# Performance work log

Measured on AMD Instinct MI355X. Metric: run time of the kernel, lower is better.

## Reference

```python
import jax, jax.numpy as jnp
import numpy as np

DIM = 300
VOCAB = 50000
B = 16
T_ART = 2000   # divisible by lcm(1,2,4,10,25)=100 -> no remainder branch in ContractExpand
T_Q = 30
T_OPT = 16
RANGES = (1, 2, 4, 10, 25)


def setup_inputs():
    key = jax.random.key(0)
    ks = jax.random.split(key, 32)
    s = 1.0 / np.sqrt(DIM)
    n = lambda i, shape, scale: jax.random.normal(ks[i], shape, jnp.float32) * scale
    return {
        "option1_in": jax.random.randint(ks[0], (B, T_OPT), 0, VOCAB),
        "option2_in": jax.random.randint(ks[1], (B, T_OPT), 0, VOCAB),
        "option3_in": jax.random.randint(ks[2], (B, T_OPT), 0, VOCAB),
        "option4_in": jax.random.randint(ks[3], (B, T_OPT), 0, VOCAB),
        "question_in": jax.random.randint(ks[4], (B, T_Q), 0, VOCAB),
        "article_in": jax.random.randint(ks[5], (B, T_ART), 0, VOCAB),
        "emb": n(6, (VOCAB, DIM), 0.1),
        # ContractExpand: 5 range-specific DIM->DIM linears
        "ce_W": n(7, (5, DIM, DIM), s),
        "ce_b": n(8, (5, DIM), 0.01),
        # MultiRangedReasoning gate mixers: 5->3 and 3->1
        "mr1_W": n(9, (3, 5), 0.4),
        "mr1_b": n(10, (3,), 0.01),
        "mr2_W": n(11, (1, 3), 0.05),   # small scale keeps gate < 1 so 2000-step scan is stable
        "mr2_b": jnp.zeros((1,), jnp.float32),
        # MRU encoding linears
        "Wz": n(12, (DIM, DIM), s), "bz": n(13, (DIM,), 0.01),
        "Wo": n(14, (DIM, DIM), s), "bo": n(15, (DIM,), 0.01),
        # BiAttention key projections
        "f1_W": n(16, (DIM, DIM), s), "f1_b": n(17, (DIM,), 0.01),
        "f2_W": n(18, (DIM, DIM), s), "f2_b": n(19, (DIM,), 0.01),
        "f3_W": n(20, (DIM, DIM), s), "f3_b": n(21, (DIM,), 0.01),
        # AnswerSelection: 2*DIM -> DIM/4 -> 1
        "as1_W": n(22, (DIM // 4, 2 * DIM), 1.0 / np.sqrt(2 * DIM)),
        "as1_b": n(23, (DIM // 4,), 0.01),
        "as2_W": n(24, (1, DIM // 4), 1.0 / np.sqrt(DIM // 4)),
        "as2_b": n(25, (1,), 0.01),
    }


def _attention(main, attn_in, W, b):
    # score[b,t,w] = (W @ attn_in[b,w] + b) . main[b,t]; softmax over w; mix attn_in
    keys = attn_in @ W.T + b                               # (B,Tw,D)
    probs = jax.nn.softmax(jnp.einsum('btd,bwd->btw', main, keys), axis=-1)
    return jnp.einsum('btw,bwd->btd', probs, attn_in)      # (B,Tt,D)


def _forward(option1_in, option2_in, option3_in, option4_in, question_in, article_in,
             emb, ce_W, ce_b, mr1_W, mr1_b, mr2_W, mr2_b, Wz, bz, Wo, bo,
             f1_W, f1_b, f2_W, f2_b, f3_W, f3_b, as1_W, as1_b, as2_W, as2_b):
    art = emb[article_in]                                  # (B,T,D)
    q = emb[question_in]                                   # (B,Tq,D)
    opts = [emb[o] for o in (option1_in, option2_in, option3_in, option4_in)]

    # --- MultiRangedReasoning gate ---
    blocks = []
    for i, r in enumerate(RANGES):
        g = T_ART // r
        xs = art.reshape(B, g, r, DIM).sum(2)              # group-sum over r consecutive words
        h = jax.nn.relu(jnp.einsum('bgd,ed->bge', xs, ce_W[i]) + ce_b[i])
        blocks.append(jnp.repeat(h, r, axis=1) / r)        # expand back to (B,T,D)
    Y = jnp.stack(blocks, axis=-1)                         # (B,T,D,5)
    h1 = jax.nn.relu(jnp.einsum('btdr,kr->btdk', Y, mr1_W) + mr1_b)
    gate = jax.nn.relu(jnp.einsum('btdk,ok->btdo', h1, mr2_W) + mr2_b)[..., 0]  # (B,T,D)

    # --- MRU encoding: c_t = g_t*c_{t-1} + (1-g_t)*z_t ; h_t = o_t*c_t ---
    z = jnp.tanh(art @ Wz.T + bz)
    o = jnp.tanh(art @ Wo.T + bo)

    def step(c, gz):
        g_t, z_t = gz
        c = g_t * c + (1.0 - g_t) * z_t
        return c, c

    _, cs = jax.lax.scan(step, jnp.zeros((B, DIM), art.dtype),
                         (gate.transpose(1, 0, 2), z.transpose(1, 0, 2)))
    art_enc = o * cs.transpose(1, 0, 2)                    # (B,T,D)

    # --- bi-attention + per-option answer vector ---
    aoq = _attention(art_enc, q, f1_W, f1_b)               # article on question
    vecs = []
    for opt in opts:
        aoqo = _attention(aoq, opt, f2_W, f2_b)            # (B,T,D)
        ooa = _attention(aoq, opt, f3_W, f3_b)             # (B,T,D)
        vecs.append(jnp.concatenate([aoqo.mean(1), ooa.mean(1)], axis=-1))  # (B,2D)
    ans = jnp.stack(vecs, 0)                               # (4,B,2D)

    h = jax.nn.relu(ans @ as1_W.T + as1_b)                 # (4,B,75)
    scores = (h @ as2_W.T + as2_b)[..., 0]                 # (4,B)
    return scores.T                                        # (B,4)


def reference(option1_in, option2_in, option3_in, option4_in, question_in, article_in,
              emb, ce_W, ce_b, mr1_W, mr1_b, mr2_W, mr2_b, Wz, bz, Wo, bo,
              f1_W, f1_b, f2_W, f2_b, f3_W, f3_b, as1_W, as1_b, as2_W, as2_b):
    return _forward(option1_in, option2_in, option3_in, option4_in, question_in, article_in,
                    emb, ce_W, ce_b, mr1_W, mr1_b, mr2_W, mr2_b, Wz, bz, Wo, bo,
                    f1_W, f1_b, f2_W, f2_b, f3_W, f3_b, as1_W, as1_b, as2_W, as2_b)
```

## Files before the change

kernel.cpp:

```cpp
#include <hip/hip_runtime.h>
#include <math.h>

typedef unsigned short ushortT;
typedef short bf8 __attribute__((ext_vector_type(8)));
typedef float f32x4 __attribute__((ext_vector_type(4)));
typedef unsigned short us4 __attribute__((ext_vector_type(4)));

__device__ __forceinline__ float bf2f(ushortT u){
    union { unsigned int i; float f; } v; v.i = ((unsigned int)u) << 16; return v.f;
}
__device__ __forceinline__ ushortT f2bf(float f){
    union { float f; unsigned int i; } v; v.f = f;
    unsigned int x = v.i;
    return (ushortT)((x + 0x7fffu + ((x >> 16) & 1u)) >> 16);
}
__device__ __forceinline__ float4 f4add(float4 a, float4 b){
    return make_float4(a.x + b.x, a.y + b.y, a.z + b.z, a.w + b.w);
}


constexpr size_t OFF_ART   = 0;
constexpr size_t OFF_R2    = 9600000;
constexpr size_t OFF_GATE  = 19200000;
constexpr size_t OFF_HC    = 28800000;
constexpr size_t OFF_WB    = 37344000;
constexpr size_t OFF_QEMB  = 38316800;
constexpr size_t OFF_KEYSQ = 38460800;
constexpr size_t OFF_OPTE  = 38604800;
constexpr size_t OFF_KEYS2 = 38912000;
constexpr size_t OFF_KEYS3 = 39219200;
constexpr size_t OFF_SCANA = 39526400;
constexpr size_t OFF_SCANB = 39718400;
constexpr size_t OFF_CST   = 39910400;
constexpr size_t OFF_PART  = 40102400;
constexpr size_t OFF_MALL  = 40231424;



__global__ void k_pack(float* ws, const float* ceW, const float* Wz, const float* Wo,
                       const float* f1W, const float* f2W, const float* f3W){
    int id = blockIdx.x * 256 + threadIdx.x;
    if (id >= 972800) return;
    int m = id / 97280; int rr = id % 97280;
    int kt = rr / 9728; rr %= 9728;
    int nt = rr / 512;  rr %= 512;
    int lane = rr / 8; int j = rr % 8;
    int d = kt * 32 + (lane >> 4) * 8 + j;
    int e = nt * 16 + (lane & 15);
    float w = 0.f;
    if (d < 300 && e < 300) {
        const float* src = (m < 5) ? (ceW + (size_t)m * 90000)
                         : (m == 5) ? Wz : (m == 6) ? Wo
                         : (m == 7) ? f1W : (m == 8) ? f2W : f3W;
        w = src[(size_t)e * 300 + d];
    }
    ushortT hi = f2bf(w);
    ushortT lo = f2bf(w - bf2f(hi));
    ushortT* wb = (ushortT*)(ws + OFF_WB);
    wb[((size_t)(m * 20 + kt) * 19 + nt) * 512 + lane * 8 + j] = hi;
    wb[((size_t)(m * 20 + 10 + kt) * 19 + nt) * 512 + lane * 8 + j] = lo;
}

__device__ __forceinline__ bf8 load_bfrag(const ushortT* wb, int mp, int kt, int nt, int lane){
    return *(const bf8*)(wb + (((size_t)(mp + kt) * 19 + nt) * 512 + lane * 8));
}
__device__ __forceinline__ bf8 lds_afrag(const ushortT* LA, int tile, int kt, int part, int lane){
    return *(const bf8*)(LA + ((tile * 10 + kt) * 2 + part) * 512 + lane * 8);
}
__device__ __forceinline__ void lds_store_split(ushortT* LA, int r, int dc4, float4 s){
    int kt = dc4 / 8;
    int kk = (dc4 % 8) * 4;
    int quad = kk / 8, j = kk % 8;
    int lane = quad * 16 + (r & 15), tile = r >> 4;
    us4 h, l;
    h.x = f2bf(s.x); l.x = f2bf(s.x - bf2f(h.x));
    h.y = f2bf(s.y); l.y = f2bf(s.y - bf2f(h.y));
    h.z = f2bf(s.z); l.z = f2bf(s.z - bf2f(h.z));
    h.w = f2bf(s.w); l.w = f2bf(s.w - bf2f(h.w));
    int base = ((tile * 10 + kt) * 2) * 512 + lane * 8 + j;
    *(us4*)&LA[base] = h;
    *(us4*)&LA[base + 512] = l;
}
__device__ __forceinline__ void lds_zero_kt9(ushortT* LA, int tid){
    for (int i = tid; i < 1024; i += 256) {
        int sl = i >> 8, u = i & 255;
        int slice = (sl < 2) ? (18 + sl) : (36 + sl);
        *(unsigned int*)&LA[slice * 512 + u * 2] = 0u;
    }
}

__global__ __launch_bounds__(320) void k_gather2(float* ws, const float* emb,
                         const int* art_in, const int* q_in,
                         const int* o1, const int* o2, const int* o3, const int* o4){
    int gb = blockIdx.x, tid = threadIdx.x;
    const float4* embv = (const float4*)emb;
    if (gb < 160) {
        if (tid >= 300) return;
        int b = gb / 10, c = gb % 10;
        int rg = tid / 75, d4 = tid % 75;
        int tbase = c * 200 + rg * 50;
        float4 s2 = make_float4(0.f,0.f,0.f,0.f), s5 = s2;
        float4* artv  = (float4*)(ws + OFF_ART);
        float4* s2v   = (float4*)(ws + OFF_GATE);
        float4* s5v   = (float4*)(ws + OFF_R2);
        for (int i = 0; i < 50; i++) {
            int t = tbase + i;
            int tok = art_in[b * 2000 + t];
            float4 v = embv[(size_t)tok * 75 + d4];
            artv[((size_t)b * 2000 + t) * 75 + d4] = v;
            s2 = f4add(s2, v); s5 = f4add(s5, v);
            if ((i & 1) == 1) { s2v[((size_t)b * 1000 + (t >> 1)) * 75 + d4] = s2; s2 = make_float4(0.f,0.f,0.f,0.f); }
            if (i % 5 == 4)   { s5v[((size_t)b * 400 + t / 5) * 75 + d4] = s5;   s5 = make_float4(0.f,0.f,0.f,0.f); }
        }
    } else {
        int id = (gb - 160) * 320 + tid;
        if (id < 36000) {
            size_t row = id / 75; int wi = id % 75;
            ((float4*)(ws + OFF_QEMB))[id] = embv[(size_t)q_in[row] * 75 + wi];
        } else if (id < 112800) {
            int i3 = id - 36000; size_t row = i3 / 75; int wi = i3 % 75;
            int opt = (int)(row / 256); int rr = (int)(row % 256);
            const int* op = (opt == 0) ? o1 : (opt == 1) ? o2 : (opt == 2) ? o3 : o4;
            ((float4*)(ws + OFF_OPTE))[i3] = embv[(size_t)op[rr] * 75 + wi];
        }
    }
}

__global__ __launch_bounds__(256) void k_ce_coarse(float* ws, const float* ceb){
    int gb = blockIdx.x;
    int kind, rows0, wi, rowLocal0;
    if (gb < 40)       { kind = 3; rows0 = 27200; wi = 4; rowLocal0 = gb * 32; }
    else if (gb < 140) { kind = 2; rows0 = 24000; wi = 3; rowLocal0 = (gb - 40) * 32; }
    else if (gb < 390) { kind = 1; rows0 = 16000; wi = 2; rowLocal0 = (gb - 140) * 32; }
    else               { kind = 0; rows0 = 0;     wi = 1; rowLocal0 = (gb - 390) * 32; }

    __shared__ ushortT LA[20480];
    int tid = threadIdx.x;
    lds_zero_kt9(LA, tid);
    __syncthreads();
    const float4* S2v = (const float4*)(ws + OFF_GATE);
    const float4* S5v = (const float4*)(ws + OFF_R2);
    for (int v = tid; v < 2400; v += 256) {
        int r = v / 75, dc4 = v % 75;
        int R = rowLocal0 + r;
        float4 s;
        if (kind == 0) {
            s = S2v[(size_t)R * 75 + dc4];
        } else if (kind == 1) {
            int b = R / 500, g = R % 500;
            const float4* p = S2v + ((size_t)b * 1000 + 2 * g) * 75 + dc4;
            s = f4add(p[0], p[75]);
        } else if (kind == 2) {
            int b = R / 200, g = R % 200;
            const float4* p = S5v + ((size_t)b * 400 + 2 * g) * 75 + dc4;
            s = f4add(p[0], p[75]);
        } else {
            int b = R / 80, g = R % 80;
            const float4* p = S5v + ((size_t)b * 400 + 5 * g) * 75 + dc4;
            s = f4add(f4add(p[0], p[75]), f4add(p[150], p[225]));
            s = f4add(s, p[300]);
        }
        lds_store_split(LA, r, dc4, s);
    }
    __syncthreads();

    int lane = tid & 63, wv = tid >> 6;
    int mrow = lane & 15, quad = lane >> 4;
    const ushortT* wb = (const ushortT*)(ws + OFF_WB);
    int mpH = wi * 20, mpL = wi * 20 + 10;

    for (int p = 0; p < 5; p++) {
        int nt = wv + p * 4; if (nt >= 19) break;
        f32x4 a0 = {0.f,0.f,0.f,0.f}, a1 = {0.f,0.f,0.f,0.f};
        #pragma unroll
        for (int kt = 0; kt < 10; kt++) {
            bf8 Ah0 = lds_afrag(LA, 0, kt, 0, lane), Al0 = lds_afrag(LA, 0, kt, 1, lane);
            bf8 Ah1 = lds_afrag(LA, 1, kt, 0, lane), Al1 = lds_afrag(LA, 1, kt, 1, lane);
            bf8 Bh = load_bfrag(wb, mpH, kt, nt, lane);
            bf8 Bl = load_bfrag(wb, mpL, kt, nt, lane);
            a0 = __builtin_amdgcn_mfma_f32_16x16x32_bf16(Ah0, Bh, a0, 0, 0, 0);
            a1 = __builtin_amdgcn_mfma_f32_16x16x32_bf16(Ah1, Bh, a1, 0, 0, 0);
            a0 = __builtin_amdgcn_mfma_f32_16x16x32_bf16(Ah0, Bl, a0, 0, 0, 0);
            a1 = __builtin_amdgcn_mfma_f32_16x16x32_bf16(Ah1, Bl, a1, 0, 0, 0);
            a0 = __builtin_amdgcn_mfma_f32_16x16x32_bf16(Al0, Bh, a0, 0, 0, 0);
            a1 = __builtin_amdgcn_mfma_f32_16x16x32_bf16(Al1, Bh, a1, 0, 0, 0);
        }
        int e = nt * 16 + mrow;
        if (e < 300) {
            float bv = ceb[wi * 300 + e];
            #pragma unroll
            for (int q = 0; q < 4; q++) {
                int r0 = rows0 + rowLocal0 + quad * 4 + q;
                ws[OFF_HC + (size_t)r0 * 300 + e] = fmaxf(a0[q] + bv, 0.f);
                ws[OFF_HC + (size_t)(r0 + 16) * 300 + e] = fmaxf(a1[q] + bv, 0.f);
            }
        }
    }
}

__global__ __launch_bounds__(256) void k_fused(float* ws, const float* ceb,
                                               const float* m1W, const float* m1b,
                                               const float* m2W, const float* m2b,
                                               const float* bz, const float* bo){
    int row0 = blockIdx.x * 32;
    __shared__ ushortT LA[20480];
    int tid = threadIdx.x;
    lds_zero_kt9(LA, tid);
    __syncthreads();
    for (int v = tid; v < 2400; v += 256) {
        int r = v / 75, dc4 = v % 75;
        float4 s = *(const float4*)&ws[OFF_ART + (size_t)(row0 + r) * 300 + dc4 * 4];
        lds_store_split(LA, r, dc4, s);
    }
    __syncthreads();

    float w1[3][5], b1[3], w2[3], b2;
    #pragma unroll
    for (int k = 0; k < 3; k++) {
        #pragma unroll
        for (int i = 0; i < 5; i++) w1[k][i] = m1W[k * 5 + i];
        b1[k] = m1b[k]; w2[k] = m2W[k];
    }
    b2 = m2b[0];

    int lane = tid & 63, wv = tid >> 6;
    int mrow = lane & 15, quad = lane >> 4;
    const ushortT* wb = (const ushortT*)(ws + OFF_WB);

    for (int p = 0; p < 5; p++) {
        int nt = wv + p * 4; if (nt >= 19) break;
        f32x4 aA0 = {0.f,0.f,0.f,0.f}, aA1 = aA0;
        f32x4 aZ0 = aA0, aZ1 = aA0, aO0 = aA0, aO1 = aA0;
        #pragma unroll
        for (int kt = 0; kt < 10; kt++) {
            bf8 Ah0 = lds_afrag(LA, 0, kt, 0, lane), Al0 = lds_afrag(LA, 0, kt, 1, lane);
            bf8 Ah1 = lds_afrag(LA, 1, kt, 0, lane), Al1 = lds_afrag(LA, 1, kt, 1, lane);
            bf8 BAh = load_bfrag(wb, 0,   kt, nt, lane);
            bf8 BAl = load_bfrag(wb, 10,  kt, nt, lane);
            bf8 BZh = load_bfrag(wb, 100, kt, nt, lane);
            bf8 BZl = load_bfrag(wb, 110, kt, nt, lane);
            bf8 BOh = load_bfrag(wb, 120, kt, nt, lane);
            bf8 BOl = load_bfrag(wb, 130, kt, nt, lane);
            aA0 = __builtin_amdgcn_mfma_f32_16x16x32_bf16(Ah0, BAh, aA0, 0, 0, 0);
            aZ0 = __builtin_amdgcn_mfma_f32_16x16x32_bf16(Ah0, BZh, aZ0, 0, 0, 0);
            aO0 = __builtin_amdgcn_mfma_f32_16x16x32_bf16(Ah0, BOh, aO0, 0, 0, 0);
            aA1 = __builtin_amdgcn_mfma_f32_16x16x32_bf16(Ah1, BAh, aA1, 0, 0, 0);
            aZ1 = __builtin_amdgcn_mfma_f32_16x16x32_bf16(Ah1, BZh, aZ1, 0, 0, 0);
            aO1 = __builtin_amdgcn_mfma_f32_16x16x32_bf16(Ah1, BOh, aO1, 0, 0, 0);
            aA0 = __builtin_amdgcn_mfma_f32_16x16x32_bf16(Ah0, BAl, aA0, 0, 0, 0);
            aZ0 = __builtin_amdgcn_mfma_f32_16x16x32_bf16(Ah0, BZl, aZ0, 0, 0, 0);
            aO0 = __builtin_amdgcn_mfma_f32_16x16x32_bf16(Ah0, BOl, aO0, 0, 0, 0);
            aA1 = __builtin_amdgcn_mfma_f32_16x16x32_bf16(Ah1, BAl, aA1, 0, 0, 0);
            aZ1 = __builtin_amdgcn_mfma_f32_16x16x32_bf16(Ah1, BZl, aZ1, 0, 0, 0);
            aO1 = __builtin_amdgcn_mfma_f32_16x16x32_bf16(Ah1, BOl, aO1, 0, 0, 0);
            aA0 = __builtin_amdgcn_mfma_f32_16x16x32_bf16(Al0, BAh, aA0, 0, 0, 0);
            aZ0 = __builtin_amdgcn_mfma_f32_16x16x32_bf16(Al0, BZh, aZ0, 0, 0, 0);
            aO0 = __builtin_amdgcn_mfma_f32_16x16x32_bf16(Al0, BOh, aO0, 0, 0, 0);
            aA1 = __builtin_amdgcn_mfma_f32_16x16x32_bf16(Al1, BAh, aA1, 0, 0, 0);
            aZ1 = __builtin_amdgcn_mfma_f32_16x16x32_bf16(Al1, BZh, aZ1, 0, 0, 0);
            aO1 = __builtin_amdgcn_mfma_f32_16x16x32_bf16(Al1, BOh, aO1, 0, 0, 0);
        }
        int e = nt * 16 + mrow;
        if (e < 300) {
            float cebe = ceb[e], bze = bz[e], boe = bo[e];
            #pragma unroll
            for (int tile = 0; tile < 2; tile++) {
                #pragma unroll
                for (int q = 0; q < 4; q++) {
                    float vA = tile ? aA1[q] : aA0[q];
                    float vZ = tile ? aZ1[q] : aZ0[q];
                    float vO = tile ? aO1[q] : aO0[q];
                    int row = row0 + tile * 16 + quad * 4 + q;
                    int bb = row / 2000, t = row % 2000;
                    size_t c1 = OFF_HC + ((size_t)bb * 1000 + t / 2) * 300;
                    size_t c2 = OFF_HC + (16000 + (size_t)bb * 500 + t / 4) * 300;
                    size_t c3 = OFF_HC + (24000 + (size_t)bb * 200 + t / 10) * 300;
                    size_t c4 = OFF_HC + (27200 + (size_t)bb * 80 + t / 25) * 300;
                    float y0 = fmaxf(vA + cebe, 0.f);
                    float y1 = ws[c1 + e] * 0.5f;
                    float y2 = ws[c2 + e] * 0.25f;
                    float y3 = ws[c3 + e] * 0.1f;
                    float y4 = ws[c4 + e] * 0.04f;
                    float gacc = b2;
                    #pragma unroll
                    for (int k = 0; k < 3; k++) {
                        float a = b1[k] + y0 * w1[k][0] + y1 * w1[k][1] + y2 * w1[k][2]
                                + y3 * w1[k][3] + y4 * w1[k][4];
                        gacc += fmaxf(a, 0.f) * w2[k];
                    }
                    ws[OFF_GATE + (size_t)row * 300 + e] = fmaxf(gacc, 0.f);
                    ws[OFF_R2 + (size_t)row * 300 + e] = tanhf(vZ + bze);
                    ws[OFF_ART + (size_t)row * 300 + e] = tanhf(vO + boe);
                }
            }
        }
    }
}

__global__ void k_scan1(float* ws){
    int tid = blockIdx.x * 256 + threadIdx.x;
    if (tid >= 192000) return;
    int c = tid / 4800, ch = tid % 4800;
    int b = ch / 300, d = ch % 300;
    size_t base = (size_t)b * 2000 * 300 + d;
    float A = 1.f, Bv = 0.f;
    int t0 = c * 50;
    for (int k = 0; k < 50; k++) {
        size_t ix = base + (size_t)(t0 + k) * 300;
        float g = ws[OFF_GATE + ix], zz = ws[OFF_R2 + ix];
        Bv = g * Bv + (1.f - g) * zz;
        A *= g;
    }
    ws[OFF_SCANA + tid] = A;
    ws[OFF_SCANB + tid] = Bv;
}

__global__ void k_scan2(float* ws){
    int ch = blockIdx.x * 256 + threadIdx.x;
    if (ch >= 4800) return;
    float c = 0.f;
    for (int j = 0; j < 40; j++) {
        ws[OFF_CST + (size_t)j * 4800 + ch] = c;
        c = ws[OFF_SCANA + (size_t)j * 4800 + ch] * c + ws[OFF_SCANB + (size_t)j * 4800 + ch];
    }
}

__global__ void k_scan3(float* ws){
    int tid = blockIdx.x * 256 + threadIdx.x;
    if (tid >= 192000) return;
    int c = tid / 4800, ch = tid % 4800;
    int b = ch / 300, d = ch % 300;
    size_t base = (size_t)b * 2000 * 300 + d;
    float cc = ws[OFF_CST + tid];
    int t0 = c * 50;
    for (int k = 0; k < 50; k++) {
        size_t ix = base + (size_t)(t0 + k) * 300;
        float g = ws[OFF_GATE + ix], zz = ws[OFF_R2 + ix];
        cc = g * cc + (1.f - g) * zz;
        ws[OFF_R2 + ix] = ws[OFF_ART + ix] * cc;
    }
}

__global__ __launch_bounds__(256) void k_keysm(float* ws, const float* f1b,
                                               const float* f2b, const float* f3b){
    int gb = blockIdx.x;
    int wm, rowLocal0; size_t inoff, outoff; const float* bias;
    if (gb < 15)      { wm = 7; inoff = OFF_QEMB; outoff = OFF_KEYSQ; bias = f1b; rowLocal0 = gb * 32; }
    else if (gb < 47) { wm = 8; inoff = OFF_OPTE; outoff = OFF_KEYS2; bias = f2b; rowLocal0 = (gb - 15) * 32; }
    else              { wm = 9; inoff = OFF_OPTE; outoff = OFF_KEYS3; bias = f3b; rowLocal0 = (gb - 47) * 32; }

    __shared__ ushortT LA[20480];
    int tid = threadIdx.x;
    lds_zero_kt9(LA, tid);
    __syncthreads();
    for (int v = tid; v < 2400; v += 256) {
        int r = v / 75, dc4 = v % 75;
        float4 s = *(const float4*)&ws[inoff + (size_t)(rowLocal0 + r) * 300 + dc4 * 4];
        lds_store_split(LA, r, dc4, s);
    }
    __syncthreads();

    int lane = tid & 63, wv = tid >> 6;
    int mrow = lane & 15, quad = lane >> 4;
    const ushortT* wb = (const ushortT*)(ws + OFF_WB);
    int mpH = wm * 20, mpL = wm * 20 + 10;

    for (int p = 0; p < 5; p++) {
        int nt = wv + p * 4; if (nt >= 19) break;
        f32x4 a0 = {0.f,0.f,0.f,0.f}, a1 = {0.f,0.f,0.f,0.f};
        #pragma unroll
        for (int kt = 0; kt < 10; kt++) {
            bf8 Ah0 = lds_afrag(LA, 0, kt, 0, lane), Al0 = lds_afrag(LA, 0, kt, 1, lane);
            bf8 Ah1 = lds_afrag(LA, 1, kt, 0, lane), Al1 = lds_afrag(LA, 1, kt, 1, lane);
            bf8 Bh = load_bfrag(wb, mpH, kt, nt, lane);
            bf8 Bl = load_bfrag(wb, mpL, kt, nt, lane);
            a0 = __builtin_amdgcn_mfma_f32_16x16x32_bf16(Ah0, Bh, a0, 0, 0, 0);
            a1 = __builtin_amdgcn_mfma_f32_16x16x32_bf16(Ah1, Bh, a1, 0, 0, 0);
            a0 = __builtin_amdgcn_mfma_f32_16x16x32_bf16(Ah0, Bl, a0, 0, 0, 0);
            a1 = __builtin_amdgcn_mfma_f32_16x16x32_bf16(Ah1, Bl, a1, 0, 0, 0);
            a0 = __builtin_amdgcn_mfma_f32_16x16x32_bf16(Al0, Bh, a0, 0, 0, 0);
            a1 = __builtin_amdgcn_mfma_f32_16x16x32_bf16(Al1, Bh, a1, 0, 0, 0);
        }
        int e = nt * 16 + mrow;
        if (e < 300) {
            float bv = bias[e];
            #pragma unroll
            for (int q = 0; q < 4; q++) {
                int r0 = rowLocal0 + quad * 4 + q;
                ws[outoff + (size_t)r0 * 300 + e] = a0[q] + bv;
                ws[outoff + (size_t)(r0 + 16) * 300 + e] = a1[q] + bv;
            }
        }
    }
}

__global__ __launch_bounds__(256) void k_matt(float* ws){
    int b = blockIdx.x;
    __shared__ float Q[30 * 300];
    int tid = threadIdx.x;
    for (int v = tid; v < 2250; v += 256)
        *(float4*)&Q[v * 4] = *(const float4*)&ws[OFF_QEMB + (size_t)b * 9000 + (size_t)v * 4];
    __syncthreads();
    int cw = tid & 127, half = tid >> 7;
    int combo = cw >> 4, w = cw & 15;
    size_t kbase = (combo < 4)
        ? OFF_KEYS2 + ((size_t)combo * 256 + (size_t)b * 16 + w) * 300
        : OFF_KEYS3 + ((size_t)(combo - 4) * 256 + (size_t)b * 16 + w) * 300;
    const float4* kr = (const float4*)&ws[kbase];
    for (int wp = half * 15; wp < half * 15 + 15; wp++) {
        const float4* qr = (const float4*)&Q[wp * 300];
        float a = 0.f;
        #pragma unroll 5
        for (int j = 0; j < 75; j++) {
            float4 k = kr[j], q = qr[j];
            a += k.x * q.x + k.y * q.y + k.z * q.z + k.w * q.w;
        }
        ws[OFF_MALL + (size_t)b * 3840 + (size_t)wp * 128 + cw] = a;
    }
}

__global__ __launch_bounds__(256) void k_attn(float* ws){
    int tile = blockIdx.x, b = blockIdx.y;
    int t0 = tile * 32;
    __shared__ __align__(16) float U[9728];
    __shared__ float S[32 * 30];
    int tid = threadIdx.x;

    for (int v = tid; v < 2432; v += 256) {
        int r = v / 76, c = v % 76;
        int t = t0 + r;
        float4 val = make_float4(0.f, 0.f, 0.f, 0.f);
        if (c < 75 && t < 2000)
            val = *(const float4*)&ws[OFF_R2 + ((size_t)b * 2000 + t) * 300 + (size_t)c * 4];
        *(float4*)&U[r * 304 + c * 4] = val;
    }
    __syncthreads();

    if (tid < 240) {
        int q = tid / 30, w = tid % 30;
        const float4* kr = (const float4*)&ws[OFF_KEYSQ + (size_t)b * 9000 + (size_t)w * 300];
        const float4* x0 = (const float4*)&U[(q * 4 + 0) * 304];
        const float4* x1 = (const float4*)&U[(q * 4 + 1) * 304];
        const float4* x2 = (const float4*)&U[(q * 4 + 2) * 304];
        const float4* x3 = (const float4*)&U[(q * 4 + 3) * 304];
        float a0 = 0.f, a1 = 0.f, a2 = 0.f, a3 = 0.f;
        #pragma unroll 5
        for (int j = 0; j < 75; j++) {
            float4 k = kr[j];
            float4 v0 = x0[j], v1 = x1[j], v2 = x2[j], v3 = x3[j];
            a0 += v0.x * k.x + v0.y * k.y + v0.z * k.z + v0.w * k.w;
            a1 += v1.x * k.x + v1.y * k.y + v1.z * k.z + v1.w * k.w;
            a2 += v2.x * k.x + v2.y * k.y + v2.z * k.z + v2.w * k.w;
            a3 += v3.x * k.x + v3.y * k.y + v3.z * k.z + v3.w * k.w;
        }
        S[(q * 4 + 0) * 30 + w] = a0;
        S[(q * 4 + 1) * 30 + w] = a1;
        S[(q * 4 + 2) * 30 + w] = a2;
        S[(q * 4 + 3) * 30 + w] = a3;
    }
    __syncthreads();

    for (int v = tid; v < 960; v += 256)
        *(float4*)&U[v * 4] = *(const float4*)&ws[OFF_MALL + (size_t)b * 3840 + (size_t)v * 4];
    if (tid < 32) {
        float m = -1e30f;
        for (int w = 0; w < 30; w++) m = fmaxf(m, S[tid * 30 + w]);
        float s = 0.f;
        for (int w = 0; w < 30; w++) { float e = expf(S[tid * 30 + w] - m); S[tid * 30 + w] = e; s += e; }
        float inv = 1.f / s;
        for (int w = 0; w < 30; w++) S[tid * 30 + w] *= inv;
    }
    __syncthreads();

    {
        int c = tid >> 5, tl = tid & 31;
        float v[16];
        #pragma unroll
        for (int w = 0; w < 16; w++) v[w] = 0.f;
        for (int wp = 0; wp < 30; wp++) {
            float p1 = S[tl * 30 + wp];
            const float* Mr = &U[wp * 128 + c * 16];
            #pragma unroll
            for (int w = 0; w < 16; w++) v[w] += p1 * Mr[w];
        }
        float mx = v[0];
        #pragma unroll
        for (int w = 1; w < 16; w++) mx = fmaxf(mx, v[w]);
        float sum = 0.f;
        #pragma unroll
        for (int w = 0; w < 16; w++) { v[w] = expf(v[w] - mx); sum += v[w]; }
        float inv = ((t0 + tl) < 2000) ? (1.f / sum) : 0.f;
        #pragma unroll
        for (int w = 0; w < 16; w += 4) {
            float4 o = make_float4(v[w] * inv, v[w+1] * inv, v[w+2] * inv, v[w+3] * inv);
            *(float4*)&U[4224 + tl * 132 + c * 16 + w] = o;
        }
    }
    __syncthreads();

    if (tid < 128) {
        int combo = tid >> 4, w = tid & 15;
        float s = 0.f;
        for (int r = 0; r < 32; r++) s += U[4224 + r * 132 + tid];
        ws[OFF_PART + (((size_t)combo * 16 + b) * 63 + tile) * 16 + w] = s;
    }
}

__global__ __launch_bounds__(256) void k_final(float* ws, const float* as1W, const float* as1b,
                                               const float* as2W, const float* as2b, float* out){
    int blk = blockIdx.x; int o = blk >> 4, b = blk & 15;
    __shared__ float vec[600]; __shared__ float cm[32]; __shared__ float hb[80];
    int tid = threadIdx.x;
    if (tid < 32) {
        int half = tid / 16, wk = tid % 16;
        int combo = half ? (4 + o) : o;
        float s = 0.f;
        size_t base = OFF_PART + (((size_t)combo * 16 + b) * 63) * 16 + wk;
        for (int t = 0; t < 63; t++) s += ws[base + (size_t)t * 16];
        cm[tid] = s * (1.f / 2000.f);
    }
    __syncthreads();
    const float* oe = ws + OFF_OPTE + ((size_t)o * 256 + (size_t)b * 16) * 300;
    for (int idx = tid; idx < 600; idx += 256) {
        int half = idx / 300, e = idx % 300;
        float acc = 0.f;
        for (int w = 0; w < 16; w++) acc += cm[half * 16 + w] * oe[(size_t)w * 300 + e];
        vec[idx] = acc;
    }
    __syncthreads();
    if (tid < 75) {
        float acc = as1b[tid];
        for (int m = 0; m < 600; m++) acc += vec[m] * as1W[(size_t)tid * 600 + m];
        hb[tid] = fmaxf(acc, 0.f);
    }
    __syncthreads();
    if (tid == 0) {
        float s = as2b[0];
        for (int j = 0; j < 75; j++) s += hb[j] * as2W[j];
        out[b * 4 + o] = s;
    }
}

extern "C" void kernel_launch(void* const* d_in, const int* in_sizes, int n_in,
                              void* d_out, int out_size, void* d_ws, size_t ws_size,
                              hipStream_t stream) {
    float* ws = (float*)d_ws;
    const int* o1 = (const int*)d_in[0];
    const int* o2 = (const int*)d_in[1];
    const int* o3 = (const int*)d_in[2];
    const int* o4 = (const int*)d_in[3];
    const int* qin = (const int*)d_in[4];
    const int* ain = (const int*)d_in[5];
    const float* emb  = (const float*)d_in[6];
    const float* ceW  = (const float*)d_in[7];
    const float* ceb  = (const float*)d_in[8];
    const float* m1W  = (const float*)d_in[9];
    const float* m1b  = (const float*)d_in[10];
    const float* m2W  = (const float*)d_in[11];
    const float* m2b  = (const float*)d_in[12];
    const float* Wz   = (const float*)d_in[13];
    const float* bz   = (const float*)d_in[14];
    const float* Wo   = (const float*)d_in[15];
    const float* bo   = (const float*)d_in[16];
    const float* f1W  = (const float*)d_in[17];
    const float* f1b  = (const float*)d_in[18];
    const float* f2W  = (const float*)d_in[19];
    const float* f2b  = (const float*)d_in[20];
    const float* f3W  = (const float*)d_in[21];
    const float* f3b  = (const float*)d_in[22];
    const float* as1W = (const float*)d_in[23];
    const float* as1b = (const float*)d_in[24];
    const float* as2W = (const float*)d_in[25];
    const float* as2b = (const float*)d_in[26];

    k_pack<<<3800, 256, 0, stream>>>(ws, ceW, Wz, Wo, f1W, f2W, f3W);
    k_gather2<<<513, 320, 0, stream>>>(ws, emb, ain, qin, o1, o2, o3, o4);
    k_ce_coarse<<<890, 256, 0, stream>>>(ws, ceb);
    k_fused<<<1000, 256, 0, stream>>>(ws, ceb, m1W, m1b, m2W, m2b, bz, bo);
    k_scan1<<<750, 256, 0, stream>>>(ws);
    k_scan2<<<19, 256, 0, stream>>>(ws);
    k_scan3<<<750, 256, 0, stream>>>(ws);
    k_keysm<<<79, 256, 0, stream>>>(ws, f1b, f2b, f3b);
    k_matt<<<16, 256, 0, stream>>>(ws);
    k_attn<<<dim3(63, 16), 256, 0, stream>>>(ws);
    k_final<<<64, 256, 0, stream>>>(ws, as1W, as1b, as2W, as2b, (float*)d_out);
}
```

Before: 539.1 us.

## Fuse scan apply into attention load, regather embeddings, finer scan chunks

The third scan pass is removed. k_attn now recomputes the recurrence for its own 32-step tile, starting from the carried state written by scan2, and multiplies by the output gate while filling shared memory. The article-embedding copy written by the gather kernel is dropped, and k_fused reads embedding rows directly through the token ids instead. Scan chunks shrink from 50 to 16 steps so that each attention tile (two chunks) lines up with a chunk boundary, and more threads run in scan1. In exchange, scan2 walks a longer serial chain, and the attention fill loop is serial over 32 timesteps with strided global loads from only 300 threads per block.

```diff
diff --git a/kernel.cpp b/kernel.cpp
--- a/kernel.cpp
+++ b/kernel.cpp
@@ -30,10 +30,10 @@
 constexpr size_t OFF_KEYS2 = 38912000;
 constexpr size_t OFF_KEYS3 = 39219200;
 constexpr size_t OFF_SCANA = 39526400;
-constexpr size_t OFF_SCANB = 39718400;
-constexpr size_t OFF_CST   = 39910400;
-constexpr size_t OFF_PART  = 40102400;
-constexpr size_t OFF_MALL  = 40231424;
+constexpr size_t OFF_SCANB = 40126400;
+constexpr size_t OFF_CST   = 40726400;
+constexpr size_t OFF_PART  = 41326400;
+constexpr size_t OFF_MALL  = 41455424;
 
 
 
@@ -100,14 +100,12 @@
         int rg = tid / 75, d4 = tid % 75;
         int tbase = c * 200 + rg * 50;
         float4 s2 = make_float4(0.f,0.f,0.f,0.f), s5 = s2;
-        float4* artv  = (float4*)(ws + OFF_ART);
-        float4* s2v   = (float4*)(ws + OFF_GATE);
-        float4* s5v   = (float4*)(ws + OFF_R2);
+        float4* s2v = (float4*)(ws + OFF_GATE);
+        float4* s5v = (float4*)(ws + OFF_R2);
         for (int i = 0; i < 50; i++) {
             int t = tbase + i;
             int tok = art_in[b * 2000 + t];
             float4 v = embv[(size_t)tok * 75 + d4];
-            artv[((size_t)b * 2000 + t) * 75 + d4] = v;
             s2 = f4add(s2, v); s5 = f4add(s5, v);
             if ((i & 1) == 1) { s2v[((size_t)b * 1000 + (t >> 1)) * 75 + d4] = s2; s2 = make_float4(0.f,0.f,0.f,0.f); }
             if (i % 5 == 4)   { s5v[((size_t)b * 400 + t / 5) * 75 + d4] = s5;   s5 = make_float4(0.f,0.f,0.f,0.f); }
@@ -198,7 +196,8 @@
     }
 }
 
-__global__ __launch_bounds__(256) void k_fused(float* ws, const float* ceb,
+__global__ __launch_bounds__(256) void k_fused(float* ws, const float* emb, const int* art_in,
+                                               const float* ceb,
                                                const float* m1W, const float* m1b,
                                                const float* m2W, const float* m2b,
                                                const float* bz, const float* bo){
@@ -207,9 +206,11 @@
     int tid = threadIdx.x;
     lds_zero_kt9(LA, tid);
     __syncthreads();
+    const float4* embv = (const float4*)emb;
     for (int v = tid; v < 2400; v += 256) {
         int r = v / 75, dc4 = v % 75;
-        float4 s = *(const float4*)&ws[OFF_ART + (size_t)(row0 + r) * 300 + dc4 * 4];
+        int tok = art_in[row0 + r];
+        float4 s = embv[(size_t)tok * 75 + dc4];
         lds_store_split(LA, r, dc4, s);
     }
     __syncthreads();
@@ -299,13 +300,13 @@
 
 __global__ void k_scan1(float* ws){
     int tid = blockIdx.x * 256 + threadIdx.x;
-    if (tid >= 192000) return;
+    if (tid >= 600000) return;
     int c = tid / 4800, ch = tid % 4800;
     int b = ch / 300, d = ch % 300;
     size_t base = (size_t)b * 2000 * 300 + d;
     float A = 1.f, Bv = 0.f;
-    int t0 = c * 50;
-    for (int k = 0; k < 50; k++) {
+    int t0 = c * 16;
+    for (int k = 0; k < 16; k++) {
         size_t ix = base + (size_t)(t0 + k) * 300;
         float g = ws[OFF_GATE + ix], zz = ws[OFF_R2 + ix];
         Bv = g * Bv + (1.f - g) * zz;
@@ -319,25 +320,9 @@
     int ch = blockIdx.x * 256 + threadIdx.x;
     if (ch >= 4800) return;
     float c = 0.f;
-    for (int j = 0; j < 40; j++) {
+    for (int j = 0; j < 125; j++) {
         ws[OFF_CST + (size_t)j * 4800 + ch] = c;
         c = ws[OFF_SCANA + (size_t)j * 4800 + ch] * c + ws[OFF_SCANB + (size_t)j * 4800 + ch];
-    }
-}
-
-__global__ void k_scan3(float* ws){
-    int tid = blockIdx.x * 256 + threadIdx.x;
-    if (tid >= 192000) return;
-    int c = tid / 4800, ch = tid % 4800;
-    int b = ch / 300, d = ch % 300;
-    size_t base = (size_t)b * 2000 * 300 + d;
-    float cc = ws[OFF_CST + tid];
-    int t0 = c * 50;
-    for (int k = 0; k < 50; k++) {
-        size_t ix = base + (size_t)(t0 + k) * 300;
-        float g = ws[OFF_GATE + ix], zz = ws[OFF_R2 + ix];
-        cc = g * cc + (1.f - g) * zz;
-        ws[OFF_R2 + ix] = ws[OFF_ART + ix] * cc;
     }
 }
 
@@ -426,13 +411,24 @@
     __shared__ float S[32 * 30];
     int tid = threadIdx.x;
 
-    for (int v = tid; v < 2432; v += 256) {
-        int r = v / 76, c = v % 76;
-        int t = t0 + r;
-        float4 val = make_float4(0.f, 0.f, 0.f, 0.f);
-        if (c < 75 && t < 2000)
-            val = *(const float4*)&ws[OFF_R2 + ((size_t)b * 2000 + t) * 300 + (size_t)c * 4];
-        *(float4*)&U[r * 304 + c * 4] = val;
+    for (int d = tid; d < 304; d += 256) {
+        if (d < 300) {
+            float cc = ws[OFF_CST + (size_t)(2 * tile) * 4800 + (size_t)b * 300 + d];
+            size_t base = (size_t)b * 2000 * 300 + d;
+            for (int i = 0; i < 32; i++) {
+                int t = t0 + i;
+                float ev = 0.f;
+                if (t < 2000) {
+                    size_t ix = base + (size_t)t * 300;
+                    float g = ws[OFF_GATE + ix], zz = ws[OFF_R2 + ix], oo = ws[OFF_ART + ix];
+                    cc = g * cc + (1.f - g) * zz;
+                    ev = oo * cc;
+                }
+                U[i * 304 + d] = ev;
+            }
+        } else {
+            for (int i = 0; i < 32; i++) U[i * 304 + d] = 0.f;
+        }
     }
     __syncthreads();
 
@@ -576,10 +572,9 @@
     k_pack<<<3800, 256, 0, stream>>>(ws, ceW, Wz, Wo, f1W, f2W, f3W);
     k_gather2<<<513, 320, 0, stream>>>(ws, emb, ain, qin, o1, o2, o3, o4);
     k_ce_coarse<<<890, 256, 0, stream>>>(ws, ceb);
-    k_fused<<<1000, 256, 0, stream>>>(ws, ceb, m1W, m1b, m2W, m2b, bz, bo);
-    k_scan1<<<750, 256, 0, stream>>>(ws);
+    k_fused<<<1000, 256, 0, stream>>>(ws, emb, ain, ceb, m1W, m1b, m2W, m2b, bz, bo);
+    k_scan1<<<2344, 256, 0, stream>>>(ws);
     k_scan2<<<19, 256, 0, stream>>>(ws);
-    k_scan3<<<750, 256, 0, stream>>>(ws);
     k_keysm<<<79, 256, 0, stream>>>(ws, f1b, f2b, f3b);
     k_matt<<<16, 256, 0, stream>>>(ws);
     k_attn<<<dim3(63, 16), 256, 0, stream>>>(ws);
```

Result: slower. 587.9 us (+9.0%).
